# Kernel optimization log

Measured on AMD Instinct MI355X. Metric: run time of the kernel, lower is better.

The kernel has to match this reference:

```python
import jax, jax.numpy as jnp
import numpy as np

B, N, T, L, H = 8, 128, 256, 32, 128


def setup_inputs() -> dict:
    key = jax.random.key(0)
    k0, k1, k2, k3, k4, k5 = jax.random.split(key, 6)
    x = jax.random.uniform(k0, (B, N, T), dtype=jnp.float32)
    s = 1.0 / np.sqrt(H)  # pytorch LSTM/Linear default init scale
    W_ih = jax.random.uniform(k1, (N, 4 * H, L), minval=-s, maxval=s, dtype=jnp.float32)
    b_ih = jax.random.uniform(k2, (N, 4 * H), minval=-s, maxval=s, dtype=jnp.float32)
    b_hh = jax.random.uniform(k3, (N, 4 * H), minval=-s, maxval=s, dtype=jnp.float32)
    W_fc = jax.random.uniform(k4, (N, N, H), minval=-s, maxval=s, dtype=jnp.float32)  # [node_i, out_j, H]
    b_fc = jax.random.uniform(k5, (N, N), minval=-s, maxval=s, dtype=jnp.float32)  # [node_i, out_j]
    return {"x": x, "W_ih": W_ih, "b_ih": b_ih, "b_hh": b_hh, "W_fc": W_fc, "b_fc": b_fc}


def reference(x, W_ih, b_ih, b_hh, W_fc, b_fc):
    # x: [B, N, T]
    Bn, Nn, Tn = x.shape
    Ln = W_ih.shape[-1]
    Hh = W_fc.shape[-1]
    Ttau = Tn - Ln  # number of prediction steps (t = L .. T-1)

    # Sliding windows x[:, i, tau:tau+L] for tau = 0..Ttau-1  -> [B, N, Ttau, L]
    idx = jnp.arange(Ttau)[:, None] + jnp.arange(Ln)[None, :]  # [Ttau, L]
    xw = x[:, :, idx]

    # Single-step LSTM with zero initial state: W_hh term vanishes.
    gates = jnp.einsum('bntl,ngl->bntg', xw, W_ih) + (b_ih + b_hh)[None, :, None, :]
    gi, gf, gg, go = jnp.split(gates, 4, axis=-1)  # pytorch order: i, f, g, o
    c = jax.nn.sigmoid(gi) * jnp.tanh(gg)          # f*c0 = 0
    h = jax.nn.sigmoid(go) * jnp.tanh(c)           # [B, N, Ttau, H]

    # Per-node fc (grouped GEMM): contributions[b, tau, j, i]
    contrib = jnp.einsum('bnth,njh->btjn', h, W_fc) + b_fc.T[None, None, :, :]

    # G[b, j, i] = mean_tau contrib[b, tau, j, i] / x[b, i, L + tau]
    denom = jnp.transpose(x[:, :, Ln:], (0, 2, 1))[:, :, None, :]  # [B, Ttau, 1, N_i]
    G = jnp.mean(contrib / denom, axis=1)                          # [B, N, N]

    X_hat = jnp.sum(contrib, axis=2) + 1e-6  # [B, Ttau, N]
    return G, X_hat
```

## Files before the change

### kernel.cpp

```cpp
#include <hip/hip_runtime.h>
#include <math.h>

#define B_  8
#define N_  128
#define T_  256
#define L_  32
#define H_  128
#define TT_ 224

typedef float f2    __attribute__((ext_vector_type(2)));
typedef float f4    __attribute__((ext_vector_type(4)));
typedef float f32x4 __attribute__((ext_vector_type(4)));
typedef short bf16x8 __attribute__((ext_vector_type(8)));

#define L2E_  1.4426950408889634f
#define L2E2_ 2.8853900817779268f

__device__ __forceinline__ unsigned pk2bf(float a, float b) {
    unsigned ua = __float_as_uint(a), ub = __float_as_uint(b);
    ua = (ua + 0x7FFFu + ((ua >> 16) & 1u)) >> 16;
    ub = (ub + 0x7FFFu + ((ub >> 16) & 1u)) >> 16;
    return ua | (ub << 16);
}
__device__ __forceinline__ float aexp2(float x) {
    float r; asm("v_exp_f32 %0, %1" : "=v"(r) : "v"(x)); return r;
}
__device__ __forceinline__ float aexp2n(float x) {
    float r; asm("v_exp_f32 %0, -%1" : "=v"(r) : "v"(x)); return r;
}
__device__ __forceinline__ float arcp(float x) {
    return __builtin_amdgcn_rcpf(x);
}

__global__ __launch_bounds__(512, 4)
void k_main(const float* __restrict__ x,
            const float* __restrict__ W_ih,
            const float* __restrict__ b_ih, const float* __restrict__ b_hh,
            const float* __restrict__ W_fc, const float* __restrict__ b_fc,
            float* __restrict__ G, float* __restrict__ xhat) {
    const int n   = blockIdx.x;
    const int b   = blockIdx.y;
    const int tid = threadIdx.x;
    const int w    = tid >> 6;
    const int lane = tid & 63;
    const int col  = lane & 15;
    const int quad = lane >> 4;

    __shared__ __attribute__((aligned(16))) float xs[260];
    __shared__ __attribute__((aligned(16))) unsigned xeo[2][128];
    __shared__ __attribute__((aligned(16))) float xr[TT_];
    __shared__ __attribute__((aligned(16))) float xh_part[8][TT_];
    __shared__ __attribute__((aligned(16))) float hd_loc[H_];
    __shared__ float red[8];
    __shared__ f4 wpart[16][32];
    __shared__ f4 ws4[32];
    __shared__ float bp[2];
    __shared__ float bs_s;

    union { uint4 u; bf16x8 v; } bfr[3];
    f32x4 biaR[3];
    {
        const int ht = w;
        const int hb = ht * 16 + quad * 4;
        #pragma unroll
        for (int g = 0; g < 3; ++g) {
            const int r  = g * 128 + ht * 16 + col;
            const int sr = r + (r >= 128 ? 128 : 0);
            const float sc = (g == 1) ? L2E2_ : L2E_;
            const f4* src = (const f4*)(W_ih + (size_t)n * 512 * L_ +
                                        (size_t)sr * L_ + quad * 8);
            f4 v0 = src[0] * sc, v1 = src[1] * sc;
            bfr[g].u.x = pk2bf(v0.x, v0.y);
            bfr[g].u.y = pk2bf(v0.z, v0.w);
            bfr[g].u.z = pk2bf(v1.x, v1.y);
            bfr[g].u.w = pk2bf(v1.z, v1.w);
            const int sg = (g == 0) ? 0 : (g == 1 ? 256 : 384);
            const f4 bi = *(const f4*)&b_ih[(size_t)n * 512 + sg + hb];
            const f4 bh = *(const f4*)&b_hh[(size_t)n * 512 + sg + hb];
            const f4 bs = (bi + bh) * sc;
            biaR[g][0] = bs.x; biaR[g][1] = bs.y;
            biaR[g][2] = bs.z; biaR[g][3] = bs.w;
        }
    }
    {
        const int h4 = tid & 31, jg = tid >> 5;
        const f4* Wf = (const f4*)(W_fc + (size_t)n * N_ * H_) +
                       (size_t)jg * 8 * 32 + h4;
        f4 s = {0.f, 0.f, 0.f, 0.f};
        #pragma unroll
        for (int j = 0; j < 8; ++j) s += Wf[j * 32];
        wpart[jg][h4] = s;
    }
    if (tid < 128) {
        float bv = b_fc[n * N_ + tid];
        #pragma unroll
        for (int off = 32; off > 0; off >>= 1) bv += __shfl_down(bv, off, 64);
        if ((tid & 63) == 0) bp[tid >> 6] = bv;
    }
    if (tid < 256) xs[tid] = x[((size_t)b * N_ + n) * T_ + tid];
    if (tid < 4)   xs[256 + tid] = 0.f;
    __syncthreads();

    if (tid < TT_) xr[tid] = 1.0f / xs[L_ + tid];
    if (tid < 128) {
        xeo[0][tid] = pk2bf(xs[2 * tid],     xs[2 * tid + 1]);
        xeo[1][tid] = pk2bf(xs[2 * tid + 1], xs[2 * tid + 2]);
    }
    if (tid < 32) {
        f4 s = wpart[0][tid];
        #pragma unroll
        for (int jg = 1; jg < 16; ++jg) s += wpart[jg][tid];
        ws4[tid] = s;
    }
    if (tid == 0) bs_s = bp[0] + bp[1];
    __syncthreads();

    const f4 wshF = ws4[(w * 16 + quad * 4) >> 2];
    const float bsum_n = bs_s;

    union { uint4 u; bf16x8 v; } af[14];
    {
        const int s0   = col + quad * 8;
        const int p    = s0 & 1;
        const int base = s0 >> 1;
        #pragma unroll
        for (int tt = 0; tt < 14; ++tt) {
            af[tt].u.x = xeo[p][tt * 8 + base + 0];
            af[tt].u.y = xeo[p][tt * 8 + base + 1];
            af[tt].u.z = xeo[p][tt * 8 + base + 2];
            af[tt].u.w = xeo[p][tt * 8 + base + 3];
        }
    }

    f32x4 hdacc = {0.f, 0.f, 0.f, 0.f};
    const f32x4 zero4 = {0.f, 0.f, 0.f, 0.f};

    #pragma unroll
    for (int ttile = 0; ttile < 14; ++ttile) {
        const float xrt = xr[ttile * 16 + col];

        f32x4 gi = __builtin_amdgcn_mfma_f32_16x16x32_bf16(bfr[0].v, af[ttile].v, zero4, 0, 0, 0);
        f32x4 gg = __builtin_amdgcn_mfma_f32_16x16x32_bf16(bfr[1].v, af[ttile].v, zero4, 0, 0, 0);
        f32x4 go = __builtin_amdgcn_mfma_f32_16x16x32_bf16(bfr[2].v, af[ttile].v, zero4, 0, 0, 0);
        gi += biaR[0];
        gg += biaR[1];
        go += biaR[2];

        f32x4 e1, e2, e3;
        #pragma unroll
        for (int r = 0; r < 4; ++r) {
            e1[r] = aexp2n(gi[r]);
            e2[r] = aexp2(gg[r]);
            e3[r] = aexp2n(go[r]);
        }
        const f32x4 A  = (1.f + e1) * (e2 + 1.f);
        const f32x4 Bv = 1.f + e3;
        const f32x4 AB = A * Bv;
        f32x4 R;
        #pragma unroll
        for (int r = 0; r < 4; ++r) R[r] = arcp(AB[r]);
        const f32x4 em = e2 - 1.f;
        const f32x4 t  = em * R;
        const f32x4 c  = t * Bv;
        const f32x4 c2 = c * c;
        f32x4 Q = c2 * -0.027698f + 0.120833f;
        Q = c2 * Q - 0.331541f;
        Q = c2 * Q + 1.0f;
        const f32x4 hh = t * Q;

        hdacc += hh * xrt;
        float xsum = fmaf(hh[0], wshF.x,
                     fmaf(hh[1], wshF.y,
                     fmaf(hh[2], wshF.z,
                     fmaf(hh[3], wshF.w, 0.f))));
        xsum += __shfl_xor(xsum, 16, 64);
        xsum += __shfl_xor(xsum, 32, 64);
        if (lane < 16) xh_part[w][ttile * 16 + lane] = xsum;
    }

    #pragma unroll
    for (int r = 0; r < 4; ++r) {
        float v = hdacc[r];
        v += __shfl_xor(v, 1, 64);
        v += __shfl_xor(v, 2, 64);
        v += __shfl_xor(v, 4, 64);
        v += __shfl_xor(v, 8, 64);
        if (col == 0) hd_loc[w * 16 + quad * 4 + r] = v;
    }
    {
        float dv = (tid < TT_) ? xr[tid] : 0.f;
        #pragma unroll
        for (int off = 32; off > 0; off >>= 1) dv += __shfl_down(dv, off, 64);
        if (lane == 0) red[w] = dv;
    }
    __syncthreads();

    if (tid < TT_) {
        const float v = (xh_part[0][tid] + xh_part[1][tid]) +
                        (xh_part[2][tid] + xh_part[3][tid]) +
                        (xh_part[4][tid] + xh_part[5][tid]) +
                        (xh_part[6][tid] + xh_part[7][tid]);
        xhat[((size_t)b * TT_ + tid) * N_ + n] = v + bsum_n + 1e-6f;
    }

    {
        const float dinv = (red[0] + red[1]) + (red[2] + red[3]) +
                           (red[4] + red[5]) + (red[6] + red[7]);
        const int j   = tid >> 2;
        const int qtr = tid & 3;
        const f4* Wf = (const f4*)(W_fc + ((size_t)n * N_ + j) * H_ + qtr * 32);
        float s = 0.f;
        #pragma unroll
        for (int q = 0; q < 8; ++q) {
            const f4 wv = Wf[q];
            const int hb = qtr * 32 + q * 4;
            s = fmaf(wv.x, hd_loc[hb + 0],
                fmaf(wv.y, hd_loc[hb + 1],
                fmaf(wv.z, hd_loc[hb + 2],
                fmaf(wv.w, hd_loc[hb + 3], s))));
        }
        s += __shfl_xor(s, 1, 64);
        s += __shfl_xor(s, 2, 64);
        if (qtr == 0) {
            const float bj = b_fc[n * N_ + j];
            G[(size_t)b * N_ * N_ + (size_t)j * N_ + n] =
                (s + bj * dinv) * (1.0f / 224.0f);
        }
    }
}

extern "C" void kernel_launch(void* const* d_in, const int* in_sizes, int n_in,
                              void* d_out, int out_size, void* d_ws, size_t ws_size,
                              hipStream_t stream) {
    const float* x    = (const float*)d_in[0];
    const float* W_ih = (const float*)d_in[1];
    const float* b_ih = (const float*)d_in[2];
    const float* b_hh = (const float*)d_in[3];
    const float* W_fc = (const float*)d_in[4];
    const float* b_fc = (const float*)d_in[5];

    float* G    = (float*)d_out;
    float* xhat = (float*)d_out + (size_t)B_ * N_ * N_;

    (void)d_ws; (void)ws_size;

    k_main<<<dim3(N_, B_), dim3(512), 0, stream>>>(x, W_ih, b_ih, b_hh,
                                                   W_fc, b_fc, G, xhat);
}
```

Measured before the change: 107.1 us.

## Process two batches per block to reuse per-node weight setup

Each block now handles two batch elements for one node, halving the grid to 512 blocks. The per-node setup (W_ih bf16 conversion, bias sums, W_fc column sums and the W_fc reads for G) is shared across both batches instead of being repeated. The MFMA/activation loop runs twice, and the A fragments are now loaded from LDS per tile rather than preloaded into registers. The cost is fewer blocks for the 256 CUs and a longer serial gate loop per block.

Result: no change. 105.6 us (-1.5%).

```diff
diff --git a/kernel.cpp b/kernel.cpp
--- a/kernel.cpp
+++ b/kernel.cpp
@@ -39,18 +39,19 @@
             const float* __restrict__ W_fc, const float* __restrict__ b_fc,
             float* __restrict__ G, float* __restrict__ xhat) {
     const int n   = blockIdx.x;
-    const int b   = blockIdx.y;
+    const int y   = blockIdx.y;
+    const int b0  = 2 * y;
     const int tid = threadIdx.x;
     const int w    = tid >> 6;
     const int lane = tid & 63;
     const int col  = lane & 15;
     const int quad = lane >> 4;
 
-    __shared__ __attribute__((aligned(16))) float xs[260];
-    __shared__ __attribute__((aligned(16))) unsigned xeo[2][128];
-    __shared__ __attribute__((aligned(16))) float xr[TT_];
-    __shared__ __attribute__((aligned(16))) float xh_part[8][TT_];
-    __shared__ __attribute__((aligned(16))) float hd_loc[H_];
+    __shared__ __attribute__((aligned(16))) float xs[2][260];
+    __shared__ __attribute__((aligned(16))) unsigned xeo[2][2][128];
+    __shared__ __attribute__((aligned(16))) float xr[2][TT_];
+    __shared__ __attribute__((aligned(16))) float xh_part[2][8][TT_];
+    __shared__ __attribute__((aligned(16))) float hd_loc[2][H_];
     __shared__ float red[8];
     __shared__ f4 wpart[16][32];
     __shared__ f4 ws4[32];
@@ -97,14 +98,20 @@
         for (int off = 32; off > 0; off >>= 1) bv += __shfl_down(bv, off, 64);
         if ((tid & 63) == 0) bp[tid >> 6] = bv;
     }
-    if (tid < 256) xs[tid] = x[((size_t)b * N_ + n) * T_ + tid];
-    if (tid < 4)   xs[256 + tid] = 0.f;
+    if (tid < 256) xs[0][tid] = x[((size_t)b0 * N_ + n) * T_ + tid];
+    else           xs[1][tid - 256] = x[((size_t)(b0 + 1) * N_ + n) * T_ + (tid - 256)];
+    if (tid < 4) { xs[0][256 + tid] = 0.f; xs[1][256 + tid] = 0.f; }
     __syncthreads();
 
-    if (tid < TT_) xr[tid] = 1.0f / xs[L_ + tid];
+    if (tid < TT_)                          xr[0][tid]       = 1.0f / xs[0][L_ + tid];
+    else if (tid >= 256 && tid < 256 + TT_) xr[1][tid - 256] = 1.0f / xs[1][L_ + tid - 256];
     if (tid < 128) {
-        xeo[0][tid] = pk2bf(xs[2 * tid],     xs[2 * tid + 1]);
-        xeo[1][tid] = pk2bf(xs[2 * tid + 1], xs[2 * tid + 2]);
+        xeo[0][0][tid] = pk2bf(xs[0][2 * tid],     xs[0][2 * tid + 1]);
+        xeo[0][1][tid] = pk2bf(xs[0][2 * tid + 1], xs[0][2 * tid + 2]);
+    } else if (tid >= 256 && tid < 384) {
+        const int t2 = tid - 256;
+        xeo[1][0][t2] = pk2bf(xs[1][2 * t2],     xs[1][2 * t2 + 1]);
+        xeo[1][1][t2] = pk2bf(xs[1][2 * t2 + 1], xs[1][2 * t2 + 2]);
     }
     if (tid < 32) {
         f4 s = wpart[0][tid];
@@ -118,113 +125,123 @@
     const f4 wshF = ws4[(w * 16 + quad * 4) >> 2];
     const float bsum_n = bs_s;
 
-    union { uint4 u; bf16x8 v; } af[14];
-    {
-        const int s0   = col + quad * 8;
-        const int p    = s0 & 1;
-        const int base = s0 >> 1;
-        #pragma unroll
-        for (int tt = 0; tt < 14; ++tt) {
-            af[tt].u.x = xeo[p][tt * 8 + base + 0];
-            af[tt].u.y = xeo[p][tt * 8 + base + 1];
-            af[tt].u.z = xeo[p][tt * 8 + base + 2];
-            af[tt].u.w = xeo[p][tt * 8 + base + 3];
-        }
-    }
-
-    f32x4 hdacc = {0.f, 0.f, 0.f, 0.f};
     const f32x4 zero4 = {0.f, 0.f, 0.f, 0.f};
+    const int p    = (col + quad * 8) & 1;
+    const int base = (col + quad * 8) >> 1;
 
     #pragma unroll
-    for (int ttile = 0; ttile < 14; ++ttile) {
-        const float xrt = xr[ttile * 16 + col];
-
-        f32x4 gi = __builtin_amdgcn_mfma_f32_16x16x32_bf16(bfr[0].v, af[ttile].v, zero4, 0, 0, 0);
-        f32x4 gg = __builtin_amdgcn_mfma_f32_16x16x32_bf16(bfr[1].v, af[ttile].v, zero4, 0, 0, 0);
-        f32x4 go = __builtin_amdgcn_mfma_f32_16x16x32_bf16(bfr[2].v, af[ttile].v, zero4, 0, 0, 0);
-        gi += biaR[0];
-        gg += biaR[1];
-        go += biaR[2];
-
-        f32x4 e1, e2, e3;
+    for (int bb = 0; bb < 2; ++bb) {
+        f32x4 hdacc = {0.f, 0.f, 0.f, 0.f};
+        #pragma unroll
+        for (int ttile = 0; ttile < 14; ++ttile) {
+            union { uint4 u; bf16x8 v; } af;
+            af.u.x = xeo[bb][p][ttile * 8 + base + 0];
+            af.u.y = xeo[bb][p][ttile * 8 + base + 1];
+            af.u.z = xeo[bb][p][ttile * 8 + base + 2];
+            af.u.w = xeo[bb][p][ttile * 8 + base + 3];
+            const float xrt = xr[bb][ttile * 16 + col];
+
+            f32x4 gi = __builtin_amdgcn_mfma_f32_16x16x32_bf16(bfr[0].v, af.v, zero4, 0, 0, 0);
+            f32x4 gg = __builtin_amdgcn_mfma_f32_16x16x32_bf16(bfr[1].v, af.v, zero4, 0, 0, 0);
+            f32x4 go = __builtin_amdgcn_mfma_f32_16x16x32_bf16(bfr[2].v, af.v, zero4, 0, 0, 0);
+            gi += biaR[0];
+            gg += biaR[1];
+            go += biaR[2];
+
+            f32x4 e1, e2, e3;
+            #pragma unroll
+            for (int r = 0; r < 4; ++r) {
+                e1[r] = aexp2n(gi[r]);
+                e2[r] = aexp2(gg[r]);
+                e3[r] = aexp2n(go[r]);
+            }
+            const f32x4 A  = (1.f + e1) * (e2 + 1.f);
+            const f32x4 Bv = 1.f + e3;
+            const f32x4 AB = A * Bv;
+            f32x4 R;
+            #pragma unroll
+            for (int r = 0; r < 4; ++r) R[r] = arcp(AB[r]);
+            const f32x4 em = e2 - 1.f;
+            const f32x4 t  = em * R;
+            const f32x4 c  = t * Bv;
+            const f32x4 c2 = c * c;
+            f32x4 Q = c2 * -0.027698f + 0.120833f;
+            Q = c2 * Q - 0.331541f;
+            Q = c2 * Q + 1.0f;
+            const f32x4 hh = t * Q;
+
+            hdacc += hh * xrt;
+            float xsum = fmaf(hh[0], wshF.x,
+                         fmaf(hh[1], wshF.y,
+                         fmaf(hh[2], wshF.z,
+                         fmaf(hh[3], wshF.w, 0.f))));
+            xsum += __shfl_xor(xsum, 16, 64);
+            xsum += __shfl_xor(xsum, 32, 64);
+            if (lane < 16) xh_part[bb][w][ttile * 16 + lane] = xsum;
+        }
         #pragma unroll
         for (int r = 0; r < 4; ++r) {
-            e1[r] = aexp2n(gi[r]);
-            e2[r] = aexp2(gg[r]);
-            e3[r] = aexp2n(go[r]);
-        }
-        const f32x4 A  = (1.f + e1) * (e2 + 1.f);
-        const f32x4 Bv = 1.f + e3;
-        const f32x4 AB = A * Bv;
-        f32x4 R;
-        #pragma unroll
-        for (int r = 0; r < 4; ++r) R[r] = arcp(AB[r]);
-        const f32x4 em = e2 - 1.f;
-        const f32x4 t  = em * R;
-        const f32x4 c  = t * Bv;
-        const f32x4 c2 = c * c;
-        f32x4 Q = c2 * -0.027698f + 0.120833f;
-        Q = c2 * Q - 0.331541f;
-        Q = c2 * Q + 1.0f;
-        const f32x4 hh = t * Q;
-
-        hdacc += hh * xrt;
-        float xsum = fmaf(hh[0], wshF.x,
-                     fmaf(hh[1], wshF.y,
-                     fmaf(hh[2], wshF.z,
-                     fmaf(hh[3], wshF.w, 0.f))));
-        xsum += __shfl_xor(xsum, 16, 64);
-        xsum += __shfl_xor(xsum, 32, 64);
-        if (lane < 16) xh_part[w][ttile * 16 + lane] = xsum;
-    }
-
-    #pragma unroll
-    for (int r = 0; r < 4; ++r) {
-        float v = hdacc[r];
-        v += __shfl_xor(v, 1, 64);
-        v += __shfl_xor(v, 2, 64);
-        v += __shfl_xor(v, 4, 64);
-        v += __shfl_xor(v, 8, 64);
-        if (col == 0) hd_loc[w * 16 + quad * 4 + r] = v;
-    }
-    {
-        float dv = (tid < TT_) ? xr[tid] : 0.f;
+            float v = hdacc[r];
+            v += __shfl_xor(v, 1, 64);
+            v += __shfl_xor(v, 2, 64);
+            v += __shfl_xor(v, 4, 64);
+            v += __shfl_xor(v, 8, 64);
+            if (col == 0) hd_loc[bb][w * 16 + quad * 4 + r] = v;
+        }
+    }
+
+    {
+        const int bb = w >> 2;
+        const int t2 = tid - bb * 256;
+        float dv = (t2 < TT_) ? xr[bb][t2] : 0.f;
         #pragma unroll
         for (int off = 32; off > 0; off >>= 1) dv += __shfl_down(dv, off, 64);
         if (lane == 0) red[w] = dv;
     }
     __syncthreads();
 
-    if (tid < TT_) {
-        const float v = (xh_part[0][tid] + xh_part[1][tid]) +
-                        (xh_part[2][tid] + xh_part[3][tid]) +
-                        (xh_part[4][tid] + xh_part[5][tid]) +
-                        (xh_part[6][tid] + xh_part[7][tid]);
-        xhat[((size_t)b * TT_ + tid) * N_ + n] = v + bsum_n + 1e-6f;
-    }
-
-    {
-        const float dinv = (red[0] + red[1]) + (red[2] + red[3]) +
-                           (red[4] + red[5]) + (red[6] + red[7]);
+    {
+        const int bb = tid >> 8;
+        const int tt = tid & 255;
+        if (tt < TT_) {
+            const float v = (xh_part[bb][0][tt] + xh_part[bb][1][tt]) +
+                            (xh_part[bb][2][tt] + xh_part[bb][3][tt]) +
+                            (xh_part[bb][4][tt] + xh_part[bb][5][tt]) +
+                            (xh_part[bb][6][tt] + xh_part[bb][7][tt]);
+            xhat[((size_t)(b0 + bb) * TT_ + tt) * N_ + n] = v + bsum_n + 1e-6f;
+        }
+    }
+
+    {
+        const float dinv0 = (red[0] + red[1]) + (red[2] + red[3]);
+        const float dinv1 = (red[4] + red[5]) + (red[6] + red[7]);
         const int j   = tid >> 2;
         const int qtr = tid & 3;
         const f4* Wf = (const f4*)(W_fc + ((size_t)n * N_ + j) * H_ + qtr * 32);
-        float s = 0.f;
+        float s0 = 0.f, s1 = 0.f;
         #pragma unroll
         for (int q = 0; q < 8; ++q) {
             const f4 wv = Wf[q];
             const int hb = qtr * 32 + q * 4;
-            s = fmaf(wv.x, hd_loc[hb + 0],
-                fmaf(wv.y, hd_loc[hb + 1],
-                fmaf(wv.z, hd_loc[hb + 2],
-                fmaf(wv.w, hd_loc[hb + 3], s))));
-        }
-        s += __shfl_xor(s, 1, 64);
-        s += __shfl_xor(s, 2, 64);
+            s0 = fmaf(wv.x, hd_loc[0][hb + 0],
+                 fmaf(wv.y, hd_loc[0][hb + 1],
+                 fmaf(wv.z, hd_loc[0][hb + 2],
+                 fmaf(wv.w, hd_loc[0][hb + 3], s0))));
+            s1 = fmaf(wv.x, hd_loc[1][hb + 0],
+                 fmaf(wv.y, hd_loc[1][hb + 1],
+                 fmaf(wv.z, hd_loc[1][hb + 2],
+                 fmaf(wv.w, hd_loc[1][hb + 3], s1))));
+        }
+        s0 += __shfl_xor(s0, 1, 64);
+        s0 += __shfl_xor(s0, 2, 64);
+        s1 += __shfl_xor(s1, 1, 64);
+        s1 += __shfl_xor(s1, 2, 64);
         if (qtr == 0) {
             const float bj = b_fc[n * N_ + j];
-            G[(size_t)b * N_ * N_ + (size_t)j * N_ + n] =
-                (s + bj * dinv) * (1.0f / 224.0f);
+            G[(size_t)b0 * N_ * N_ + (size_t)j * N_ + n] =
+                (s0 + bj * dinv0) * (1.0f / 224.0f);
+            G[(size_t)(b0 + 1) * N_ * N_ + (size_t)j * N_ + n] =
+                (s1 + bj * dinv1) * (1.0f / 224.0f);
         }
     }
 }
@@ -244,6 +261,6 @@
 
     (void)d_ws; (void)ws_size;
 
-    k_main<<<dim3(N_, B_), dim3(512), 0, stream>>>(x, W_ih, b_ih, b_hh,
-                                                   W_fc, b_fc, G, xhat);
-}
+    k_main<<<dim3(N_, B_ / 2), dim3(512), 0, stream>>>(x, W_ih, b_ih, b_hh,
+                                                       W_fc, b_fc, G, xhat);
+}
```
